# Kernel optimization log

Measured on AMD Instinct MI355X. Metric: run time of the kernel, lower is better.

The kernel has to match this reference:

```python
import jax, jax.numpy as jnp
from jax import lax
import numpy as np

B, S, E, HID = 16, 7, 64, 64
RES = (64, 64); D = RES[0] * RES[1]
XLOW, XHIGH = -0.5, 0.5
RLOW, RHIGH = float(np.sqrt(0.01)), float(np.sqrt(0.05))
PIXEL_MULT = 1.0; N_ITER = 3; TSOFT = 1.0 / float(np.sqrt(E))

def _build_grid():
    ranges = [np.linspace(XLOW, XHIGH, r) for r in RES]
    g = np.stack(np.meshgrid(*ranges, indexing='xy'), axis=-1)
    g = g.reshape(RES[0], RES[1], -1).reshape(1, -1, 2)
    return jnp.asarray(g, dtype=jnp.float32)

ABS_GRID = _build_grid()  # [1, D, 2]

def _ln(x, g, b):
    m = jnp.mean(x, -1, keepdims=True)
    v = jnp.mean(jnp.square(x - m), -1, keepdims=True)
    return (x - m) * lax.rsqrt(v + 1e-5) * g + b

def _forward(data, slot_noise, pos_rand, conv0_w, conv0_b, conv1_w, conv1_b, conv2_w, conv2_b,
             dataN_g, dataN_b, queryN_g, queryN_b, toK_w, toK_b, toV_w, toV_b, dense_w, dense_b,
             mlp1_w, mlp1_b, mlp2_w, mlp2_b, gru_wih, gru_whh, gru_bih, gru_bhh,
             alpha1_w, alpha1_b, alpha2_w, alpha2_b, final1_w, final1_b, final2_w, final2_b,
             slots_mu, slots_logsigma):
    dn = ('NCHW', 'OIHW', 'NCHW')
    def conv(x, w, b):
        return lax.conv_general_dilated(x, w, (1, 1), 'SAME', dimension_numbers=dn) + b[None, :, None, None]
    # CNN encoder: Conv-ReLU x3, 'same' padding, k=5
    x = jax.nn.relu(conv(data, conv0_w, conv0_b))
    x = jax.nn.relu(conv(x, conv1_w, conv1_b))
    x = jax.nn.relu(conv(x, conv2_w, conv2_b))
    enc = x.transpose(0, 2, 3, 1).reshape(B, D, HID)
    enc = _ln(enc, dataN_g, dataN_b)

    queries = slots_mu + jnp.exp(slots_logsigma) * slot_noise  # [B,S,E]
    # init_slots: faithful replication (source indexes the SLOT dim, and swaps rlow/rhigh)
    pos_scale = pos_rand.at[:, :2, :].add(-0.5)
    pos_scale = pos_scale.at[:, -1, :].set((RLOW - RHIGH) * pos_rand[:, -1, :] + RHIGH)

    encK = enc @ toK_w + toK_b  # [B,D,E]
    encV = enc @ toV_w + toV_b

    def init_mlp(y):
        y = _ln(y, queryN_g, queryN_b)
        return jax.nn.relu(y @ mlp1_w + mlp1_b) @ mlp2_w + mlp2_b

    def get_kv(ps):
        # per-slot relative grid: [B,S,D,2]
        rel = (ABS_GRID[:, None] - ps[:, :, None, :2]) / ps[:, :, -1][:, :, None, None]
        eg = PIXEL_MULT * (rel @ dense_w + dense_b)  # [B,S,D,E]
        return init_mlp(encK[:, None] + eg), init_mlp(encV[:, None] + eg)

    def att_wts(q, k):
        logits = jnp.einsum('bse,bsde->bsd', q, k) * TSOFT
        att = jax.nn.softmax(logits, axis=1)  # softmax over slots
        wts = att / jnp.sum(att, -1, keepdims=True) + 1e-8
        return att, wts

    def update_frames(wts):
        new_pos = jnp.einsum('bsd,de->bse', wts, ABS_GRID[0])  # [B,S,2]
        d2 = jnp.sum(jnp.square(ABS_GRID[:, None] - new_pos[:, :, None]), -1)  # [B,S,D]
        new_scale = jnp.sqrt(jnp.einsum('bsd,bsd->bs', wts, d2))
        return jnp.concatenate([new_pos, new_scale[..., None]], -1)

    def gru(xg, h):
        gi = xg @ gru_wih.T + gru_bih
        gh = h @ gru_whh.T + gru_bhh
        ir, iz, inn = jnp.split(gi, 3, -1)
        hr, hz, hn = jnp.split(gh, 3, -1)
        r = jax.nn.sigmoid(ir + hr)
        z = jax.nn.sigmoid(iz + hz)
        n = jnp.tanh(inn + r * hn)
        return (1.0 - z) * n + z * h

    for _ in range(N_ITER):
        keys, vals = get_kv(pos_scale)
        att, wts = att_wts(_ln(queries, queryN_g, queryN_b), keys)
        pos_scale = update_frames(wts)
        upd = jnp.einsum('bsd,bsde->bse', wts, vals)
        queries = gru(upd.reshape(-1, E), queries.reshape(-1, E)).reshape(B, S, E)

    keys, _ = get_kv(pos_scale)
    att, wts = att_wts(_ln(queries, queryN_g, queryN_b), keys)
    nps = update_frames(wts)
    alpha = jax.nn.sigmoid(jax.nn.relu(queries @ alpha1_w + alpha1_b) @ alpha2_w + alpha2_b)
    slot_feat = jax.nn.relu(queries @ final1_w + final1_b) @ final2_w + final2_b + nps
    return queries, att, slot_feat, alpha

def setup_inputs() -> dict:
    ks = jax.random.split(jax.random.key(0), 20)
    f32 = jnp.float32
    def rn(i, shape, s):
        return jax.random.normal(ks[i], shape, f32) * s
    inp = dict(
        data=jax.random.normal(ks[0], (B, 1, RES[0], RES[1]), f32),
        slot_noise=jax.random.normal(ks[1], (B, S, E), f32),
        pos_rand=jax.random.uniform(ks[2], (B, S, 3), dtype=f32),
        conv0_w=rn(3, (HID, 1, 5, 5), 0.2), conv0_b=jnp.zeros(HID, f32),
        conv1_w=rn(4, (HID, HID, 5, 5), 0.025), conv1_b=jnp.zeros(HID, f32),
        conv2_w=rn(5, (HID, HID, 5, 5), 0.025), conv2_b=jnp.zeros(HID, f32),
        dataN_g=jnp.ones(HID, f32), dataN_b=jnp.zeros(HID, f32),
        queryN_g=jnp.ones(E, f32), queryN_b=jnp.zeros(E, f32),
        toK_w=rn(6, (HID, E), 0.125), toK_b=jnp.zeros(E, f32),
        toV_w=rn(7, (HID, E), 0.125), toV_b=jnp.zeros(E, f32),
        dense_w=rn(8, (2, E), 0.7), dense_b=jnp.zeros(E, f32),
        mlp1_w=rn(9, (E, E), 0.125), mlp1_b=jnp.zeros(E, f32),
        mlp2_w=rn(10, (E, E), 0.125), mlp2_b=jnp.zeros(E, f32),
        gru_wih=rn(11, (3 * E, E), 0.125), gru_whh=rn(12, (3 * E, E), 0.125),
        gru_bih=jnp.zeros(3 * E, f32), gru_bhh=jnp.zeros(3 * E, f32),
        alpha1_w=rn(13, (E, 32), 0.125), alpha1_b=jnp.zeros(32, f32),
        alpha2_w=rn(14, (32, 1), 0.18), alpha2_b=jnp.zeros(1, f32),
        final1_w=rn(15, (E, HID), 0.125), final1_b=jnp.zeros(HID, f32),
        final2_w=rn(16, (HID, 3), 0.125), final2_b=jnp.zeros(3, f32),
        slots_mu=rn(17, (1, 1, E), 1.0),
        slots_logsigma=rn(18, (1, 1, E), 0.01),
    )
    return inp

def reference(data, slot_noise, pos_rand, conv0_w, conv0_b, conv1_w, conv1_b, conv2_w, conv2_b,
              dataN_g, dataN_b, queryN_g, queryN_b, toK_w, toK_b, toV_w, toV_b, dense_w, dense_b,
              mlp1_w, mlp1_b, mlp2_w, mlp2_b, gru_wih, gru_whh, gru_bih, gru_bhh,
              alpha1_w, alpha1_b, alpha2_w, alpha2_b, final1_w, final1_b, final2_w, final2_b,
              slots_mu, slots_logsigma):
    return _forward(data, slot_noise, pos_rand, conv0_w, conv0_b, conv1_w, conv1_b, conv2_w, conv2_b,
                    dataN_g, dataN_b, queryN_g, queryN_b, toK_w, toK_b, toV_w, toV_b, dense_w, dense_b,
                    mlp1_w, mlp1_b, mlp2_w, mlp2_b, gru_wih, gru_whh, gru_bih, gru_bhh,
                    alpha1_w, alpha1_b, alpha2_w, alpha2_b, final1_w, final1_b, final2_w, final2_b,
                    slots_mu, slots_logsigma)
```

## Files before the change

### kernel.cpp

```cpp
#include <hip/hip_runtime.h>
#include <cmath>


#define RLOW_F 0.1f
#define RHIGH_F 0.22360679774997896f
#define W0CONST 1.00004096f
#define SR2 704.3386243f

typedef __attribute__((ext_vector_type(8))) __bf16 bf16x8;
typedef __attribute__((ext_vector_type(4))) float f32x4;

__device__ __forceinline__ float wsum64(float v){
  #pragma unroll
  for (int off = 32; off > 0; off >>= 1) v += __shfl_xor(v, off, 64);
  return v;
}
__device__ __forceinline__ float rdlane(float v, int l){
  return __int_as_float(__builtin_amdgcn_readlane(__float_as_int(v), l));
}
__device__ __forceinline__ unsigned short bf16bits(float v){
  __bf16 h = (__bf16)v;
  return *reinterpret_cast<unsigned short*>(&h);
}

__device__ __forceinline__ void pp_core(int row, int e, float qv,
    float px, float py, float sc,
    const float* __restrict__ qg_, const float* __restrict__ qb_,
    const float* __restrict__ dw, const float* __restrict__ db,
    const float* __restrict__ mlp2w, const float* __restrict__ mlp2b,
    float* __restrict__ absc, float* __restrict__ w2qc){
  float m = wsum64(qv) * (1.f/64.f);
  float d = qv - m;
  float var = wsum64(d*d) * (1.f/64.f);
  float qlnv = d * (1.0f/sqrtf(var + 1e-5f)) * qg_[e] + qb_[e];
  float A  = dw[e]      / sc;
  float Bv = dw[64 + e] / sc;
  absc[row*192 + e]       = A;
  absc[row*192 + 64 + e]  = Bv;
  absc[row*192 + 128 + e] = db[e] - px*A - py*Bv;
  float acc = 0.f;
  const float* wrow = mlp2w + e*64;
  for (int j = 0; j < 64; j++) acc = fmaf(wrow[j], rdlane(qlnv, j), acc);
  w2qc[row*68 + e] = acc;
  float c2 = wsum64(mlp2b[e] * qlnv);
  if (e == 0) w2qc[row*68 + 64] = c2;
}

__global__ void k_prep(const float* __restrict__ noise, const float* __restrict__ prand,
                       const float* __restrict__ mu, const float* __restrict__ logsig,
                       const float* __restrict__ qg_, const float* __restrict__ qb_,
                       const float* __restrict__ dw, const float* __restrict__ db,
                       const float* __restrict__ mlp2w, const float* __restrict__ mlp2b,
                       float* __restrict__ queries, float* __restrict__ ps,
                       float* __restrict__ absc, float* __restrict__ w2qc,
                       float* __restrict__ accF, float* __restrict__ upd){
  int row = blockIdx.x;
  int e = threadIdx.x;
  int s = row % 7;
  float qv = mu[e] + expf(logsig[e]) * noise[row*64 + e];
  queries[row*64 + e] = qv;
  upd[row*64 + e] = 0.f;
  if (e < 4) accF[row*4 + e] = 0.f;
  float pv = 0.f;
  if (e < 3){
    float pr = prand[row*3 + e];
    if (s < 2)       pv = pr - 0.5f;
    else if (s == 6) pv = (RLOW_F - RHIGH_F)*pr + RHIGH_F;
    else             pv = pr;
    ps[row*3 + e] = pv;
  }
  float px = rdlane(pv, 0), py = rdlane(pv, 1), sc = rdlane(pv, 2);
  pp_core(row, e, qv, px, py, sc, qg_, qb_, dw, db, mlp2w, mlp2b, absc, w2qc);
}

__global__ __launch_bounds__(256) void k_conv0(const float* __restrict__ in,
                        const float* __restrict__ w, const float* __restrict__ bias,
                        unsigned short* __restrict__ out){
  int bi = blockIdx.x; int b = bi >> 6; int y = bi & 63;
  int t = threadIdx.x; int lane = t & 63; int xg = t >> 6;
  __shared__ float s_in[5*68];
  __shared__ float s_w[64*25];
  __shared__ float s_out[64*65];
  for (int i = t; i < 1600; i += 256) s_w[i] = w[i];
  for (int i = t; i < 340; i += 256){
    int r = i / 68, cx = i % 68;
    int yy = y + r - 2, gx = cx - 2;
    float v = 0.f;
    if (yy >= 0 && yy < 64 && gx >= 0 && gx < 64) v = in[(b*64 + yy)*64 + gx];
    s_in[r*68 + cx] = v;
  }
  __syncthreads();
  int o = lane;
  float bvv = bias[o];
  float acc[16];
  #pragma unroll
  for (int k = 0; k < 16; k++) acc[k] = bvv;
  #pragma unroll
  for (int ky = 0; ky < 5; ky++){
    float rv[20];
    const float4* p = reinterpret_cast<const float4*>(&s_in[ky*68 + xg*16]);
    #pragma unroll
    for (int q = 0; q < 5; q++){ float4 f = p[q]; rv[q*4]=f.x; rv[q*4+1]=f.y; rv[q*4+2]=f.z; rv[q*4+3]=f.w; }
    #pragma unroll
    for (int kx = 0; kx < 5; kx++){
      float wv = s_w[o*25 + ky*5 + kx];
      #pragma unroll
      for (int k = 0; k < 16; k++) acc[k] = fmaf(rv[k+kx], wv, acc[k]);
    }
  }
  #pragma unroll
  for (int k = 0; k < 16; k++) s_out[o*65 + xg*16 + k] = fmaxf(acc[k], 0.f);
  __syncthreads();
  for (int i = t; i < 4096; i += 256){
    int px = i >> 6, ch = i & 63;
    out[((size_t)(b*64 + y)*64 + px)*64 + ch] = bf16bits(s_out[ch*65 + px]);
  }
}

__global__ void k_packconv(const float* __restrict__ w, unsigned short* __restrict__ out){
  int idx = blockIdx.x*256 + threadIdx.x;
  if (idx >= 102400) return;
  int j = idx & 7;
  int l = (idx >> 3) & 63;
  int frag = idx >> 9;
  int nt = frag & 3;
  int ks = (frag >> 2) % 10;
  int dy = frag / 40;
  int q = l >> 4, cr = l & 15;
  int k = ks*32 + q*8 + j;
  int kx = k >> 6, ch = k & 63;
  int n = nt*16 + cr;
  out[idx] = bf16bits(w[((n*64 + ch)*5 + dy)*5 + kx]);
}

__global__ __launch_bounds__(256) void k_convm(const unsigned short* __restrict__ in_bf,
                        const unsigned short* __restrict__ wpack,
                        const float* __restrict__ bias,
                        const float* __restrict__ lng, const float* __restrict__ lnb,
                        unsigned short* __restrict__ out_bf, float* __restrict__ out_f,
                        int mode){
  int bi = blockIdx.x;
  int b = bi >> 4; int yg = bi & 15;
  int t = threadIdx.x; int wv = t >> 6; int l = t & 63;
  int q = l >> 4, cr = l & 15;
  int p0 = wv*16;

  __shared__ char lds[8*68*144];

  for (int ri = 0; ri < 8; ri++){
    int yy = yg*4 + ri - 2;
    bool rok = (yy >= 0 && yy < 64);
    const uint4* src = reinterpret_cast<const uint4*>(in_bf + (size_t)(b*64 + yy)*64*64);
    for (int i = t; i < 544; i += 256){
      int px = i >> 3, c8 = i & 7;
      uint4 v = {0u,0u,0u,0u};
      int gx = px - 2;
      if (rok && gx >= 0 && gx < 64) v = src[gx*8 + c8];
      *reinterpret_cast<uint4*>(&lds[ri*9792 + px*144 + c8*16]) = v;
    }
  }
  __syncthreads();

  f32x4 acc[4][4];
  #pragma unroll
  for (int r = 0; r < 4; r++)
    #pragma unroll
    for (int nt = 0; nt < 4; nt++) acc[r][nt] = (f32x4){0.f,0.f,0.f,0.f};

  const bf16x8* wp = reinterpret_cast<const bf16x8*>(wpack);
  for (int dy = 0; dy < 5; dy++){
    for (int ks = 0; ks < 10; ks++){
      bf16x8 Bf[4];
      int fbase = (dy*10 + ks)*4;
      #pragma unroll
      for (int nt = 0; nt < 4; nt++) Bf[nt] = wp[(fbase + nt)*64 + l];
      int aoff = (p0 + cr + (ks >> 1))*144 + (ks & 1)*64 + q*16;
      #pragma unroll
      for (int r = 0; r < 4; r++){
        bf16x8 a = *reinterpret_cast<const bf16x8*>(&lds[(r + dy)*9792 + aoff]);
        #pragma unroll
        for (int nt = 0; nt < 4; nt++)
          acc[r][nt] = __builtin_amdgcn_mfma_f32_16x16x32_bf16(a, Bf[nt], acc[r][nt], 0, 0, 0);
      }
    }
  }

  float bvv[4];
  #pragma unroll
  for (int nt = 0; nt < 4; nt++) bvv[nt] = bias[nt*16 + cr];

  if (mode == 0){
    #pragma unroll
    for (int r = 0; r < 4; r++){
      int y = yg*4 + r;
      #pragma unroll
      for (int reg = 0; reg < 4; reg++){
        int p = p0 + q*4 + reg;
        size_t base = ((size_t)(b*64 + y)*64 + p)*64;
        #pragma unroll
        for (int nt = 0; nt < 4; nt++)
          out_bf[base + nt*16 + cr] = bf16bits(fmaxf(acc[r][nt][reg] + bvv[nt], 0.f));
      }
    }
  } else {
    float gv[4], bb[4];
    #pragma unroll
    for (int nt = 0; nt < 4; nt++){ gv[nt] = lng[nt*16 + cr]; bb[nt] = lnb[nt*16 + cr]; }
    #pragma unroll
    for (int r = 0; r < 4; r++){
      int y = yg*4 + r;
      #pragma unroll
      for (int reg = 0; reg < 4; reg++){
        int p = p0 + q*4 + reg;
        float v[4]; float s1 = 0.f, s2 = 0.f;
        #pragma unroll
        for (int nt = 0; nt < 4; nt++){
          v[nt] = fmaxf(acc[r][nt][reg] + bvv[nt], 0.f);
          s1 += v[nt]; s2 += v[nt]*v[nt];
        }
        #pragma unroll
        for (int m = 1; m < 16; m <<= 1){ s1 += __shfl_xor(s1, m, 64); s2 += __shfl_xor(s2, m, 64); }
        float mean = s1 * (1.f/64.f);
        float var  = s2 * (1.f/64.f) - mean*mean;
        float rstd = 1.0f/sqrtf(var + 1e-5f);
        size_t base = ((size_t)b*4096 + y*64 + p)*64;
        #pragma unroll
        for (int nt = 0; nt < 4; nt++)
          out_f[base + nt*16 + cr] = (v[nt] - mean)*rstd*gv[nt] + bb[nt];
      }
    }
  }
}

__global__ void k_packw1(const float* __restrict__ w1, unsigned short* __restrict__ out){
  int idx = blockIdx.x*256 + threadIdx.x;
  int jj = idx & 7;
  int lane = (idx >> 3) & 63;
  int frag = idx >> 9;
  int ks = frag >> 2, nt = frag & 3;
  int q = lane >> 4, cr = lane & 15;
  int k = ks*32 + q*8 + jj;
  int n = nt*16 + cr;
  out[idx] = bf16bits(w1[k*64 + n]);
}

__global__ __launch_bounds__(256) void k_projm(const float* __restrict__ enc,
                       const unsigned short* __restrict__ kpack, const float* __restrict__ bk,
                       const unsigned short* __restrict__ vpack, const float* __restrict__ bvp,
                       unsigned short* __restrict__ K, unsigned short* __restrict__ V){
  int bi = blockIdx.x; int b = bi >> 6; int tile = bi & 63;
  int t = threadIdx.x; int wv = t >> 6; int l = t & 63;
  int q = l >> 4, cr = l & 15;
  int d0 = tile*64 + wv*16;

  const bf16x8* kp = reinterpret_cast<const bf16x8*>(kpack);
  const bf16x8* vp = reinterpret_cast<const bf16x8*>(vpack);
  bf16x8 KB[8], VB[8];
  #pragma unroll
  for (int f = 0; f < 8; f++){ KB[f] = kp[f*64 + l]; VB[f] = vp[f*64 + l]; }

  const float* er = enc + (size_t)(b*4096 + d0 + cr)*64;
  bf16x8 a0, a1;
  #pragma unroll
  for (int h = 0; h < 2; h++){
    const float4* e4 = reinterpret_cast<const float4*>(er + (h ? (32 + q*8) : (q*8)));
    #pragma unroll
    for (int p = 0; p < 2; p++){
      float4 e = e4[p];
      if (h == 0){ a0[p*4+0]=(__bf16)e.x; a0[p*4+1]=(__bf16)e.y; a0[p*4+2]=(__bf16)e.z; a0[p*4+3]=(__bf16)e.w; }
      else       { a1[p*4+0]=(__bf16)e.x; a1[p*4+1]=(__bf16)e.y; a1[p*4+2]=(__bf16)e.z; a1[p*4+3]=(__bf16)e.w; }
    }
  }

  f32x4 zero = {0.f,0.f,0.f,0.f};
  f32x4 aK[4], aV[4];
  #pragma unroll
  for (int nt = 0; nt < 4; nt++){
    aK[nt] = __builtin_amdgcn_mfma_f32_16x16x32_bf16(a0, KB[nt],     zero,   0, 0, 0);
    aK[nt] = __builtin_amdgcn_mfma_f32_16x16x32_bf16(a1, KB[4 + nt], aK[nt], 0, 0, 0);
    aV[nt] = __builtin_amdgcn_mfma_f32_16x16x32_bf16(a0, VB[nt],     zero,   0, 0, 0);
    aV[nt] = __builtin_amdgcn_mfma_f32_16x16x32_bf16(a1, VB[4 + nt], aV[nt], 0, 0, 0);
  }
  #pragma unroll
  for (int nt = 0; nt < 4; nt++){
    float bkv = bk[nt*16 + cr], bvv = bvp[nt*16 + cr];
    #pragma unroll
    for (int reg = 0; reg < 4; reg++){
      size_t base = ((size_t)b*4096 + d0 + q*4 + reg)*64 + nt*16 + cr;
      K[base] = bf16bits(aK[nt][reg] + bkv);
      V[base] = bf16bits(aV[nt][reg] + bvv);
    }
  }
}

__global__ __launch_bounds__(256) void k_attnK(const unsigned short* __restrict__ encX,
     const unsigned short* __restrict__ w1pack, const float* __restrict__ mlp1b,
     const float* __restrict__ absc, const float* __restrict__ qg_,
     const float* __restrict__ qb_, const float* __restrict__ w2qc,
     float* __restrict__ att, float* __restrict__ accF){
  int bi = blockIdx.x;
  int b = bi >> 6, tile = bi & 63;
  int t = threadIdx.x; int wv = t >> 6; int l = t & 63;
  int q = l >> 4, cr = l & 15;
  int m0 = tile*64 + wv*16;
  int drow = m0 + cr;

  __shared__ float s_log[7*64];
  __shared__ float s_absc[7*192];
  __shared__ float s_wq[7*68];
  for (int i = t; i < 1344; i += 256) s_absc[i] = absc[b*7*192 + i];
  for (int i = t; i < 476;  i += 256) s_wq[i]   = w2qc[b*7*68 + i];

  const bf16x8* wp = reinterpret_cast<const bf16x8*>(w1pack);
  bf16x8 Bf[8];
  #pragma unroll
  for (int f = 0; f < 8; f++) Bf[f] = wp[f*64 + l];

  const unsigned short* er = encX + (size_t)(b*4096 + drow)*64;
  float gx = -0.5f + (float)(drow & 63) * (1.f/63.f);
  float gy = -0.5f + (float)((drow >> 6) & 63) * (1.f/63.f);
  float xb[16], gq[16], bq[16];
  {
    bf16x8 ea = *reinterpret_cast<const bf16x8*>(er + q*8);
    bf16x8 eb = *reinterpret_cast<const bf16x8*>(er + 32 + q*8);
    #pragma unroll
    for (int i = 0; i < 8; i++){ xb[i] = (float)ea[i]; xb[8+i] = (float)eb[i]; }
  }
  #pragma unroll
  for (int h = 0; h < 2; h++){
    int fb = h ? (32 + q*8) : (q*8);
    const float4* g4 = reinterpret_cast<const float4*>(qg_ + fb);
    const float4* b4 = reinterpret_cast<const float4*>(qb_ + fb);
    #pragma unroll
    for (int p = 0; p < 2; p++){
      float4 gg = g4[p], bb = b4[p];
      int o = h*8 + p*4;
      gq[o+0]=gg.x; gq[o+1]=gg.y; gq[o+2]=gg.z; gq[o+3]=gg.w;
      bq[o+0]=bb.x; bq[o+1]=bb.y; bq[o+2]=bb.z; bq[o+3]=bb.w;
    }
  }
  float b1v[4];
  #pragma unroll
  for (int nt = 0; nt < 4; nt++) b1v[nt] = mlp1b[nt*16 + cr];
  __syncthreads();

  for (int s = 0; s < 7; s++){
    const float* Ac = s_absc + s*192;
    float x[16];
    #pragma unroll
    for (int h = 0; h < 2; h++){
      int fb = h ? (32 + q*8) : (q*8);
      const float4* A4 = reinterpret_cast<const float4*>(Ac + fb);
      const float4* B4 = reinterpret_cast<const float4*>(Ac + 64 + fb);
      const float4* C4 = reinterpret_cast<const float4*>(Ac + 128 + fb);
      #pragma unroll
      for (int p = 0; p < 2; p++){
        float4 Av = A4[p], Bv = B4[p], Cv = C4[p];
        int o = h*8 + p*4;
        x[o+0] = xb[o+0] + gx*Av.x + gy*Bv.x + Cv.x;
        x[o+1] = xb[o+1] + gx*Av.y + gy*Bv.y + Cv.y;
        x[o+2] = xb[o+2] + gx*Av.z + gy*Bv.z + Cv.z;
        x[o+3] = xb[o+3] + gx*Av.w + gy*Bv.w + Cv.w;
      }
    }
    float sum = 0.f;
    #pragma unroll
    for (int k = 0; k < 16; k++) sum += x[k];
    sum += __shfl_xor(sum, 16, 64); sum += __shfl_xor(sum, 32, 64);
    float m = sum * (1.f/64.f);
    float v = 0.f;
    #pragma unroll
    for (int k = 0; k < 16; k++){ float dd = x[k] - m; v += dd*dd; }
    v += __shfl_xor(v, 16, 64); v += __shfl_xor(v, 32, 64);
    float rstd = 1.0f/sqrtf(v * (1.f/64.f) + 1e-5f);

    bf16x8 a0, a1;
    #pragma unroll
    for (int k = 0; k < 8; k++)  a0[k] = (__bf16)((x[k]   - m)*rstd*gq[k]   + bq[k]);
    #pragma unroll
    for (int k = 0; k < 8; k++)  a1[k] = (__bf16)((x[8+k] - m)*rstd*gq[8+k] + bq[8+k]);

    f32x4 zero = {0.f, 0.f, 0.f, 0.f};
    f32x4 acc[4];
    #pragma unroll
    for (int nt = 0; nt < 4; nt++){
      acc[nt] = __builtin_amdgcn_mfma_f32_16x16x32_bf16(a0, Bf[nt],     zero,    0, 0, 0);
      acc[nt] = __builtin_amdgcn_mfma_f32_16x16x32_bf16(a1, Bf[4 + nt], acc[nt], 0, 0, 0);
    }

    float c2 = s_wq[s*68 + 64];
    float p[4] = {0.f, 0.f, 0.f, 0.f};
    #pragma unroll
    for (int nt = 0; nt < 4; nt++){
      float wqv = s_wq[s*68 + nt*16 + cr];
      #pragma unroll
      for (int reg = 0; reg < 4; reg++){
        float y = fmaxf(acc[nt][reg] + b1v[nt], 0.f);
        p[reg] = fmaf(y, wqv, p[reg]);
      }
    }
    #pragma unroll
    for (int reg = 0; reg < 4; reg++){
      #pragma unroll
      for (int off = 1; off < 16; off <<= 1) p[reg] += __shfl_xor(p[reg], off, 64);
    }
    if (cr == 0){
      #pragma unroll
      for (int reg = 0; reg < 4; reg++)
        s_log[s*64 + wv*16 + q*4 + reg] = (p[reg] + c2) * 0.125f;
    }
  }
  __syncthreads();

  if (t < 64){
    float lv[7];
    #pragma unroll
    for (int s = 0; s < 7; s++) lv[s] = s_log[s*64 + t];
    float mx = lv[0];
    #pragma unroll
    for (int s = 1; s < 7; s++) mx = fmaxf(mx, lv[s]);
    float sm = 0.f;
    #pragma unroll
    for (int s = 0; s < 7; s++){ lv[s] = expf(lv[s] - mx); sm += lv[s]; }
    float inv = 1.0f / sm;
    #pragma unroll
    for (int s = 0; s < 7; s++){
      float a = lv[s] * inv;
      s_log[s*64 + t] = a;
      att[(size_t)(b*7+s)*4096 + tile*64 + t] = a;
    }
  }
  __syncthreads();

  if (t < 224){
    int s = t >> 5, r = t & 31;
    float a1 = s_log[s*64 + r];
    float a2 = s_log[s*64 + r + 32];
    float gx1 = -0.5f + (float)r * (1.f/63.f);
    float gx2 = -0.5f + (float)(r + 32) * (1.f/63.f);
    float gyc = -0.5f + (float)tile * (1.f/63.f);
    float gy2c = gyc*gyc;
    float w0 = a1 + a2;
    float w1 = a1*gx1 + a2*gx2;
    float w2 = w0*gyc;
    float w3 = a1*(gx1*gx1 + gy2c) + a2*(gx2*gx2 + gy2c);
    #pragma unroll
    for (int m = 1; m < 32; m <<= 1){
      w0 += __shfl_xor(w0, m, 64);
      w1 += __shfl_xor(w1, m, 64);
      w2 += __shfl_xor(w2, m, 64);
      w3 += __shfl_xor(w3, m, 64);
    }
    if (r == 0){
      atomicAdd(&accF[(b*7+s)*4 + 0], w0);
      atomicAdd(&accF[(b*7+s)*4 + 1], w1);
      atomicAdd(&accF[(b*7+s)*4 + 2], w2);
      atomicAdd(&accF[(b*7+s)*4 + 3], w3);
    }
  }
}

__global__ __launch_bounds__(256) void k_attnV(const unsigned short* __restrict__ encX,
     const unsigned short* __restrict__ w1pack, const float* __restrict__ mlp1b,
     const float* __restrict__ absc, const float* __restrict__ qg_,
     const float* __restrict__ qb_, const float* __restrict__ att,
     const float* __restrict__ accF, float* __restrict__ upd){
  int bi = blockIdx.x;
  int b = bi >> 6, tile = bi & 63;
  int t = threadIdx.x; int wv = t >> 6; int l = t & 63;
  int q = l >> 4, cr = l & 15;
  int m0 = tile*64 + wv*16;
  int drow = m0 + cr;

  __shared__ float s_absc[7*192];
  __shared__ float s_att[7*64];
  __shared__ float s_upd[7*64];
  __shared__ float s_inv[7];
  for (int i = t; i < 1344; i += 256) s_absc[i] = absc[b*7*192 + i];
  for (int i = t; i < 448;  i += 256){
    s_att[i] = att[(size_t)(b*7 + (i >> 6))*4096 + tile*64 + (i & 63)];
    s_upd[i] = 0.f;
  }
  if (t < 7) s_inv[t] = 1.0f / accF[(b*7 + t)*4];

  const bf16x8* wp = reinterpret_cast<const bf16x8*>(w1pack);
  bf16x8 Bf[8];
  #pragma unroll
  for (int f = 0; f < 8; f++) Bf[f] = wp[f*64 + l];

  const unsigned short* er = encX + (size_t)(b*4096 + drow)*64;
  float gx = -0.5f + (float)(drow & 63) * (1.f/63.f);
  float gy = -0.5f + (float)((drow >> 6) & 63) * (1.f/63.f);
  float xb[16], gq[16], bq[16];
  {
    bf16x8 ea = *reinterpret_cast<const bf16x8*>(er + q*8);
    bf16x8 eb = *reinterpret_cast<const bf16x8*>(er + 32 + q*8);
    #pragma unroll
    for (int i = 0; i < 8; i++){ xb[i] = (float)ea[i]; xb[8+i] = (float)eb[i]; }
  }
  #pragma unroll
  for (int h = 0; h < 2; h++){
    int fb = h ? (32 + q*8) : (q*8);
    const float4* g4 = reinterpret_cast<const float4*>(qg_ + fb);
    const float4* b4 = reinterpret_cast<const float4*>(qb_ + fb);
    #pragma unroll
    for (int p = 0; p < 2; p++){
      float4 gg = g4[p], bb = b4[p];
      int o = h*8 + p*4;
      gq[o+0]=gg.x; gq[o+1]=gg.y; gq[o+2]=gg.z; gq[o+3]=gg.w;
      bq[o+0]=bb.x; bq[o+1]=bb.y; bq[o+2]=bb.z; bq[o+3]=bb.w;
    }
  }
  float b1v[4];
  #pragma unroll
  for (int nt = 0; nt < 4; nt++) b1v[nt] = mlp1b[nt*16 + cr];
  __syncthreads();

  for (int s = 0; s < 7; s++){
    const float* Ac = s_absc + s*192;
    float x[16];
    #pragma unroll
    for (int h = 0; h < 2; h++){
      int fb = h ? (32 + q*8) : (q*8);
      const float4* A4 = reinterpret_cast<const float4*>(Ac + fb);
      const float4* B4 = reinterpret_cast<const float4*>(Ac + 64 + fb);
      const float4* C4 = reinterpret_cast<const float4*>(Ac + 128 + fb);
      #pragma unroll
      for (int p = 0; p < 2; p++){
        float4 Av = A4[p], Bv = B4[p], Cv = C4[p];
        int o = h*8 + p*4;
        x[o+0] = xb[o+0] + gx*Av.x + gy*Bv.x + Cv.x;
        x[o+1] = xb[o+1] + gx*Av.y + gy*Bv.y + Cv.y;
        x[o+2] = xb[o+2] + gx*Av.z + gy*Bv.z + Cv.z;
        x[o+3] = xb[o+3] + gx*Av.w + gy*Bv.w + Cv.w;
      }
    }
    float sum = 0.f;
    #pragma unroll
    for (int k = 0; k < 16; k++) sum += x[k];
    sum += __shfl_xor(sum, 16, 64); sum += __shfl_xor(sum, 32, 64);
    float m = sum * (1.f/64.f);
    float v = 0.f;
    #pragma unroll
    for (int k = 0; k < 16; k++){ float dd = x[k] - m; v += dd*dd; }
    v += __shfl_xor(v, 16, 64); v += __shfl_xor(v, 32, 64);
    float rstd = 1.0f/sqrtf(v * (1.f/64.f) + 1e-5f);

    bf16x8 a0, a1;
    #pragma unroll
    for (int k = 0; k < 8; k++)  a0[k] = (__bf16)((x[k]   - m)*rstd*gq[k]   + bq[k]);
    #pragma unroll
    for (int k = 0; k < 8; k++)  a1[k] = (__bf16)((x[8+k] - m)*rstd*gq[8+k] + bq[8+k]);

    f32x4 zero = {0.f, 0.f, 0.f, 0.f};
    f32x4 acc[4];
    #pragma unroll
    for (int nt = 0; nt < 4; nt++){
      acc[nt] = __builtin_amdgcn_mfma_f32_16x16x32_bf16(a0, Bf[nt],     zero,    0, 0, 0);
      acc[nt] = __builtin_amdgcn_mfma_f32_16x16x32_bf16(a1, Bf[4 + nt], acc[nt], 0, 0, 0);
    }

    float rsa = s_inv[s];
    float wr[4];
    #pragma unroll
    for (int reg = 0; reg < 4; reg++)
      wr[reg] = fmaf(s_att[s*64 + wv*16 + q*4 + reg], rsa, 1e-8f);
    float pc[4];
    #pragma unroll
    for (int nt = 0; nt < 4; nt++){
      pc[nt] = 0.f;
      #pragma unroll
      for (int reg = 0; reg < 4; reg++)
        pc[nt] = fmaf(wr[reg], fmaxf(acc[nt][reg] + b1v[nt], 0.f), pc[nt]);
    }
    #pragma unroll
    for (int nt = 0; nt < 4; nt++){
      pc[nt] += __shfl_xor(pc[nt], 16, 64);
      pc[nt] += __shfl_xor(pc[nt], 32, 64);
    }
    if (q == 0){
      #pragma unroll
      for (int nt = 0; nt < 4; nt++)
        atomicAdd(&s_upd[s*64 + nt*16 + cr], pc[nt]);
    }
  }
  __syncthreads();
  for (int i = t; i < 448; i += 256)
    atomicAdd(&upd[b*448 + i], s_upd[i]);
}

__global__ void k_gru(float* __restrict__ upd, float* __restrict__ queries,
                      const float* __restrict__ wih, const float* __restrict__ whh,
                      const float* __restrict__ bih, const float* __restrict__ bhh,
                      const float* __restrict__ mlp2w, const float* __restrict__ mlp2b,
                      float* __restrict__ accF, float* __restrict__ ps,
                      const float* __restrict__ qg_, const float* __restrict__ qb_,
                      const float* __restrict__ dw, const float* __restrict__ db,
                      float* __restrict__ absc, float* __restrict__ w2qc){
  int row = blockIdx.x; int t = threadIdx.x;
  __shared__ float us[64], hs[64], xs[64], gis[192], ghs[192];
  __shared__ float s_ps3[3];
  if (t < 64){ us[t] = upd[row*64 + t]; hs[t] = queries[row*64 + t]; }
  if (t == 64){
    float sa = accF[row*4+0];
    float ax = accF[row*4+1], ay = accF[row*4+2], ar2 = accF[row*4+3];
    float isa = 1.0f/sa;
    float Wx = ax*isa, Wy = ay*isa;
    float Wg = ar2*isa + 1e-8f*SR2;
    float s2 = Wg - (Wx*Wx + Wy*Wy)*(2.f - W0CONST);
    s_ps3[0] = Wx; s_ps3[1] = Wy; s_ps3[2] = sqrtf(fmaxf(s2, 0.f));
  }
  __syncthreads();
  if (t < 64){
    float a = W0CONST * mlp2b[t];
    for (int i = 0; i < 64; i++) a = fmaf(us[i], mlp2w[i*64 + t], a);
    xs[t] = a;
  }
  __syncthreads();
  float gi = bih[t], gh = bhh[t];
  for (int e = 0; e < 64; e++){
    gi = fmaf(wih[t*64 + e], xs[e], gi);
    gh = fmaf(whh[t*64 + e], hs[e], gh);
  }
  gis[t] = gi; ghs[t] = gh;
  __syncthreads();
  if (t < 64){
    float r = 1.0f/(1.0f + expf(-(gis[t]      + ghs[t])));
    float z = 1.0f/(1.0f + expf(-(gis[64+t]   + ghs[64+t])));
    float n = tanhf(gis[128+t] + r*ghs[128+t]);
    float newq = (1.0f - z)*n + z*hs[t];
    queries[row*64 + t] = newq;
    upd[row*64 + t] = 0.f;
    if (t < 4) accF[row*4 + t] = 0.f;
    if (t < 3) ps[row*3 + t] = s_ps3[t];
    pp_core(row, t, newq, s_ps3[0], s_ps3[1], s_ps3[2],
            qg_, qb_, dw, db, mlp2w, mlp2b, absc, w2qc);
  }
}

__global__ void k_final(const float* __restrict__ queries, const float* __restrict__ accF,
                        const float* __restrict__ a1w, const float* __restrict__ a1b,
                        const float* __restrict__ a2w, const float* __restrict__ a2b,
                        const float* __restrict__ f1w, const float* __restrict__ f1b,
                        const float* __restrict__ f2w, const float* __restrict__ f2b,
                        float* __restrict__ out){
  int bs = blockIdx.x; int e = threadIdx.x;
  __shared__ float qs[64], hf[64], ha[32];
  float q = queries[bs*64 + e];
  qs[e] = q;
  out[bs*64 + e] = q;
  __syncthreads();
  float accf = f1b[e];
  for (int i = 0; i < 64; i++) accf = fmaf(qs[i], f1w[i*64 + e], accf);
  hf[e] = fmaxf(accf, 0.f);
  if (e < 32){
    float acca = a1b[e];
    for (int i = 0; i < 64; i++) acca = fmaf(qs[i], a1w[i*32 + e], acca);
    ha[e] = fmaxf(acca, 0.f);
  }
  __syncthreads();
  if (e < 3){
    float sf = f2b[e];
    for (int o = 0; o < 64; o++) sf = fmaf(hf[o], f2w[o*3 + e], sf);
    float sa = accF[bs*4+0], ax = accF[bs*4+1], ay = accF[bs*4+2], ar2 = accF[bs*4+3];
    float isa = 1.0f/sa;
    float Wx = ax*isa, Wy = ay*isa;
    float Wg = ar2*isa + 1e-8f*SR2;
    float s2 = Wg - (Wx*Wx + Wy*Wy)*(2.f - W0CONST);
    float nv = (e == 0) ? Wx : ((e == 1) ? Wy : sqrtf(fmaxf(s2, 0.f)));
    out[465920 + bs*3 + e] = sf + nv;
  }
  if (e == 32){
    float al = a2b[0];
    for (int o = 0; o < 32; o++) al = fmaf(ha[o], a2w[o], al);
    out[466256 + bs] = 1.0f/(1.0f + expf(-al));
  }
}

extern "C" void kernel_launch(void* const* d_in, const int* in_sizes, int n_in,
                              void* d_out, int out_size, void* d_ws, size_t ws_size,
                              hipStream_t stream){
  const float* data        = (const float*)d_in[0];
  const float* slot_noise  = (const float*)d_in[1];
  const float* pos_rand    = (const float*)d_in[2];
  const float* conv0_w     = (const float*)d_in[3];
  const float* conv0_b     = (const float*)d_in[4];
  const float* conv1_w     = (const float*)d_in[5];
  const float* conv1_b     = (const float*)d_in[6];
  const float* conv2_w     = (const float*)d_in[7];
  const float* conv2_b     = (const float*)d_in[8];
  const float* dataN_g     = (const float*)d_in[9];
  const float* dataN_b     = (const float*)d_in[10];
  const float* queryN_g    = (const float*)d_in[11];
  const float* queryN_b    = (const float*)d_in[12];
  const float* toK_w       = (const float*)d_in[13];
  const float* toK_b       = (const float*)d_in[14];
  const float* toV_w       = (const float*)d_in[15];
  const float* toV_b       = (const float*)d_in[16];
  const float* dense_w     = (const float*)d_in[17];
  const float* dense_b     = (const float*)d_in[18];
  const float* mlp1_w      = (const float*)d_in[19];
  const float* mlp1_b      = (const float*)d_in[20];
  const float* mlp2_w      = (const float*)d_in[21];
  const float* mlp2_b      = (const float*)d_in[22];
  const float* gru_wih     = (const float*)d_in[23];
  const float* gru_whh     = (const float*)d_in[24];
  const float* gru_bih     = (const float*)d_in[25];
  const float* gru_bhh     = (const float*)d_in[26];
  const float* alpha1_w    = (const float*)d_in[27];
  const float* alpha1_b    = (const float*)d_in[28];
  const float* alpha2_w    = (const float*)d_in[29];
  const float* alpha2_b    = (const float*)d_in[30];
  const float* final1_w    = (const float*)d_in[31];
  const float* final1_b    = (const float*)d_in[32];
  const float* final2_w    = (const float*)d_in[33];
  const float* final2_b    = (const float*)d_in[34];
  const float* slots_mu    = (const float*)d_in[35];
  const float* slots_lsig  = (const float*)d_in[36];

  float* ws   = (float*)d_ws;
  float* bufA = ws;
  float* bufB = bufA + 4194304;
  float* bufC = bufB + 4194304;
  float* attw = bufC + 4194304;
  float* queries = attw + 458752;
  float* ps   = queries + 7168;
  float* absc = ps + 512;
  float* accF = absc + 21504;
  float* upd  = accF + 512;
  float* w2qc = upd + 7168;
  unsigned short* w1pack = (unsigned short*)(w2qc + 7616);
  unsigned short* kpack  = w1pack + 4096;
  unsigned short* vpack  = kpack + 4096;
  unsigned short* wp1    = vpack + 4096;
  unsigned short* wp2    = wp1 + 102400;

  unsigned short* c0_bf = (unsigned short*)bufA;
  unsigned short* c1_bf = (unsigned short*)bufC;
  float* enc = bufB;
  unsigned short* encK = (unsigned short*)bufA;
  unsigned short* encV = (unsigned short*)bufC;

  float* outq   = (float*)d_out;
  float* outatt = outq + 7168;

  k_prep<<<112, 64, 0, stream>>>(slot_noise, pos_rand, slots_mu, slots_lsig,
                                 queryN_g, queryN_b, dense_w, dense_b, mlp2_w, mlp2_b,
                                 queries, ps, absc, w2qc, accF, upd);
  k_packw1<<<16, 256, 0, stream>>>(mlp1_w, w1pack);
  k_packw1<<<16, 256, 0, stream>>>(toK_w, kpack);
  k_packw1<<<16, 256, 0, stream>>>(toV_w, vpack);
  k_packconv<<<400, 256, 0, stream>>>(conv1_w, wp1);
  k_packconv<<<400, 256, 0, stream>>>(conv2_w, wp2);
  k_conv0<<<1024, 256, 0, stream>>>(data, conv0_w, conv0_b, c0_bf);
  k_convm<<<256, 256, 0, stream>>>(c0_bf, wp1, conv1_b, nullptr, nullptr, c1_bf, nullptr, 0);
  k_convm<<<256, 256, 0, stream>>>(c1_bf, wp2, conv2_b, dataN_g, dataN_b, nullptr, enc, 1);
  k_projm<<<1024, 256, 0, stream>>>(enc, kpack, toK_b, vpack, toV_b, encK, encV);

  for (int p = 0; p < 4; p++){
    float* attp = (p == 3) ? outatt : attw;
    k_attnK<<<1024, 256, 0, stream>>>(encK, w1pack, mlp1_b, absc, queryN_g, queryN_b,
                                      w2qc, attp, accF);
    if (p < 3){
      k_attnV<<<1024, 256, 0, stream>>>(encV, w1pack, mlp1_b, absc, queryN_g, queryN_b,
                                        attp, accF, upd);
      k_gru<<<112, 192, 0, stream>>>(upd, queries, gru_wih, gru_whh, gru_bih, gru_bhh,
                                     mlp2_w, mlp2_b, accF, ps, queryN_g, queryN_b,
                                     dense_w, dense_b, absc, w2qc);
    }
  }
  k_final<<<112, 64, 0, stream>>>(queries, accF,
                                  alpha1_w, alpha1_b, alpha2_w, alpha2_b,
                                  final1_w, final1_b, final2_w, final2_b, outq);
}
```

Before: 535.2 us.

## Stage MLP1 weights in LDS and process slot pairs in attention kernels

Both attention kernels now copy the packed MLP1 weight fragments into shared memory instead of holding eight bf16x8 fragments in registers per lane. They also process two slots per loop iteration to interleave independent MFMA chains, and compute layernorm variance in a single pass from sum and sum of squares. A launch bound of 4 blocks per SM is added to push register use down for higher occupancy. The trade-offs are LDS reads per MFMA, one duplicated wasted slot computation on the final odd iteration, and slightly less numerically stable variance.

```diff
diff --git a/kernel.cpp b/kernel.cpp
--- a/kernel.cpp
+++ b/kernel.cpp
@@ -293,7 +293,7 @@
   }
 }
 
-__global__ __launch_bounds__(256) void k_attnK(const unsigned short* __restrict__ encX,
+__global__ __launch_bounds__(256, 4) void k_attnK(const unsigned short* __restrict__ encX,
      const unsigned short* __restrict__ w1pack, const float* __restrict__ mlp1b,
      const float* __restrict__ absc, const float* __restrict__ qg_,
      const float* __restrict__ qb_, const float* __restrict__ w2qc,
@@ -308,13 +308,14 @@
   __shared__ float s_log[7*64];
   __shared__ float s_absc[7*192];
   __shared__ float s_wq[7*68];
+  __shared__ unsigned short s_w1[4096];
   for (int i = t; i < 1344; i += 256) s_absc[i] = absc[b*7*192 + i];
   for (int i = t; i < 476;  i += 256) s_wq[i]   = w2qc[b*7*68 + i];
-
-  const bf16x8* wp = reinterpret_cast<const bf16x8*>(w1pack);
-  bf16x8 Bf[8];
-  #pragma unroll
-  for (int f = 0; f < 8; f++) Bf[f] = wp[f*64 + l];
+  {
+    const uint4* g = reinterpret_cast<const uint4*>(w1pack);
+    uint4* d = reinterpret_cast<uint4*>(s_w1);
+    for (int i = t; i < 512; i += 256) d[i] = g[i];
+  }
 
   const unsigned short* er = encX + (size_t)(b*4096 + drow)*64;
   float gx = -0.5f + (float)(drow & 63) * (1.f/63.f);
@@ -344,70 +345,113 @@
   for (int nt = 0; nt < 4; nt++) b1v[nt] = mlp1b[nt*16 + cr];
   __syncthreads();
 
-  for (int s = 0; s < 7; s++){
-    const float* Ac = s_absc + s*192;
-    float x[16];
-    #pragma unroll
-    for (int h = 0; h < 2; h++){
-      int fb = h ? (32 + q*8) : (q*8);
-      const float4* A4 = reinterpret_cast<const float4*>(Ac + fb);
-      const float4* B4 = reinterpret_cast<const float4*>(Ac + 64 + fb);
-      const float4* C4 = reinterpret_cast<const float4*>(Ac + 128 + fb);
-      #pragma unroll
-      for (int p = 0; p < 2; p++){
-        float4 Av = A4[p], Bv = B4[p], Cv = C4[p];
-        int o = h*8 + p*4;
-        x[o+0] = xb[o+0] + gx*Av.x + gy*Bv.x + Cv.x;
-        x[o+1] = xb[o+1] + gx*Av.y + gy*Bv.y + Cv.y;
-        x[o+2] = xb[o+2] + gx*Av.z + gy*Bv.z + Cv.z;
-        x[o+3] = xb[o+3] + gx*Av.w + gy*Bv.w + Cv.w;
-      }
-    }
-    float sum = 0.f;
-    #pragma unroll
-    for (int k = 0; k < 16; k++) sum += x[k];
-    sum += __shfl_xor(sum, 16, 64); sum += __shfl_xor(sum, 32, 64);
-    float m = sum * (1.f/64.f);
-    float v = 0.f;
-    #pragma unroll
-    for (int k = 0; k < 16; k++){ float dd = x[k] - m; v += dd*dd; }
-    v += __shfl_xor(v, 16, 64); v += __shfl_xor(v, 32, 64);
-    float rstd = 1.0f/sqrtf(v * (1.f/64.f) + 1e-5f);
-
-    bf16x8 a0, a1;
-    #pragma unroll
-    for (int k = 0; k < 8; k++)  a0[k] = (__bf16)((x[k]   - m)*rstd*gq[k]   + bq[k]);
-    #pragma unroll
-    for (int k = 0; k < 8; k++)  a1[k] = (__bf16)((x[8+k] - m)*rstd*gq[8+k] + bq[8+k]);
-
-    f32x4 zero = {0.f, 0.f, 0.f, 0.f};
-    f32x4 acc[4];
+  const bf16x8* wl = reinterpret_cast<const bf16x8*>(s_w1);
+  f32x4 zero = {0.f, 0.f, 0.f, 0.f};
+
+  for (int sp = 0; sp < 4; sp++){
+    int s0 = sp*2;
+    int np = (sp == 3) ? 1 : 2;
+    int sB = (np == 2) ? s0 + 1 : s0;
+    float x0[16], x1[16];
+    float s1a = 0.f, s2a = 0.f, s1b = 0.f, s2b = 0.f;
+    {
+      const float* Ac = s_absc + s0*192;
+      #pragma unroll
+      for (int h = 0; h < 2; h++){
+        int fb = h ? (32 + q*8) : (q*8);
+        const float4* A4 = reinterpret_cast<const float4*>(Ac + fb);
+        const float4* B4 = reinterpret_cast<const float4*>(Ac + 64 + fb);
+        const float4* C4 = reinterpret_cast<const float4*>(Ac + 128 + fb);
+        #pragma unroll
+        for (int p = 0; p < 2; p++){
+          float4 Av = A4[p], Bv = B4[p], Cv = C4[p];
+          int o = h*8 + p*4;
+          x0[o+0] = xb[o+0] + gx*Av.x + gy*Bv.x + Cv.x;
+          x0[o+1] = xb[o+1] + gx*Av.y + gy*Bv.y + Cv.y;
+          x0[o+2] = xb[o+2] + gx*Av.z + gy*Bv.z + Cv.z;
+          x0[o+3] = xb[o+3] + gx*Av.w + gy*Bv.w + Cv.w;
+        }
+      }
+      #pragma unroll
+      for (int k = 0; k < 16; k++){ s1a += x0[k]; s2a = fmaf(x0[k], x0[k], s2a); }
+    }
+    {
+      const float* Ac = s_absc + sB*192;
+      #pragma unroll
+      for (int h = 0; h < 2; h++){
+        int fb = h ? (32 + q*8) : (q*8);
+        const float4* A4 = reinterpret_cast<const float4*>(Ac + fb);
+        const float4* B4 = reinterpret_cast<const float4*>(Ac + 64 + fb);
+        const float4* C4 = reinterpret_cast<const float4*>(Ac + 128 + fb);
+        #pragma unroll
+        for (int p = 0; p < 2; p++){
+          float4 Av = A4[p], Bv = B4[p], Cv = C4[p];
+          int o = h*8 + p*4;
+          x1[o+0] = xb[o+0] + gx*Av.x + gy*Bv.x + Cv.x;
+          x1[o+1] = xb[o+1] + gx*Av.y + gy*Bv.y + Cv.y;
+          x1[o+2] = xb[o+2] + gx*Av.z + gy*Bv.z + Cv.z;
+          x1[o+3] = xb[o+3] + gx*Av.w + gy*Bv.w + Cv.w;
+        }
+      }
+      #pragma unroll
+      for (int k = 0; k < 16; k++){ s1b += x1[k]; s2b = fmaf(x1[k], x1[k], s2b); }
+    }
+    s1a += __shfl_xor(s1a, 16, 64); s2a += __shfl_xor(s2a, 16, 64);
+    s1b += __shfl_xor(s1b, 16, 64); s2b += __shfl_xor(s2b, 16, 64);
+    s1a += __shfl_xor(s1a, 32, 64); s2a += __shfl_xor(s2a, 32, 64);
+    s1b += __shfl_xor(s1b, 32, 64); s2b += __shfl_xor(s2b, 32, 64);
+    float mA = s1a*(1.f/64.f);
+    float rA = 1.0f/sqrtf(s2a*(1.f/64.f) - mA*mA + 1e-5f);
+    float mB = s1b*(1.f/64.f);
+    float rB = 1.0f/sqrtf(s2b*(1.f/64.f) - mB*mB + 1e-5f);
+
+    bf16x8 a00, a01, a10, a11;
+    #pragma unroll
+    for (int k = 0; k < 8; k++){
+      a00[k] = (__bf16)((x0[k]    - mA)*rA*gq[k]   + bq[k]);
+      a01[k] = (__bf16)((x0[8+k]  - mA)*rA*gq[8+k] + bq[8+k]);
+      a10[k] = (__bf16)((x1[k]    - mB)*rB*gq[k]   + bq[k]);
+      a11[k] = (__bf16)((x1[8+k]  - mB)*rB*gq[8+k] + bq[8+k]);
+    }
+
+    f32x4 acc0[4], acc1[4];
     #pragma unroll
     for (int nt = 0; nt < 4; nt++){
-      acc[nt] = __builtin_amdgcn_mfma_f32_16x16x32_bf16(a0, Bf[nt],     zero,    0, 0, 0);
-      acc[nt] = __builtin_amdgcn_mfma_f32_16x16x32_bf16(a1, Bf[4 + nt], acc[nt], 0, 0, 0);
-    }
-
-    float c2 = s_wq[s*68 + 64];
-    float p[4] = {0.f, 0.f, 0.f, 0.f};
+      bf16x8 w0 = wl[nt*64 + l];
+      bf16x8 w1f = wl[(4 + nt)*64 + l];
+      acc0[nt] = __builtin_amdgcn_mfma_f32_16x16x32_bf16(a00, w0,  zero,     0, 0, 0);
+      acc0[nt] = __builtin_amdgcn_mfma_f32_16x16x32_bf16(a01, w1f, acc0[nt], 0, 0, 0);
+      acc1[nt] = __builtin_amdgcn_mfma_f32_16x16x32_bf16(a10, w0,  zero,     0, 0, 0);
+      acc1[nt] = __builtin_amdgcn_mfma_f32_16x16x32_bf16(a11, w1f, acc1[nt], 0, 0, 0);
+    }
+
+    float p0[4] = {0.f,0.f,0.f,0.f}, p1[4] = {0.f,0.f,0.f,0.f};
     #pragma unroll
     for (int nt = 0; nt < 4; nt++){
-      float wqv = s_wq[s*68 + nt*16 + cr];
+      float wq0 = s_wq[s0*68 + nt*16 + cr];
+      float wq1 = s_wq[sB*68 + nt*16 + cr];
       #pragma unroll
       for (int reg = 0; reg < 4; reg++){
-        float y = fmaxf(acc[nt][reg] + b1v[nt], 0.f);
-        p[reg] = fmaf(y, wqv, p[reg]);
-      }
-    }
-    #pragma unroll
-    for (int reg = 0; reg < 4; reg++){
-      #pragma unroll
-      for (int off = 1; off < 16; off <<= 1) p[reg] += __shfl_xor(p[reg], off, 64);
+        p0[reg] = fmaf(fmaxf(acc0[nt][reg] + b1v[nt], 0.f), wq0, p0[reg]);
+        p1[reg] = fmaf(fmaxf(acc1[nt][reg] + b1v[nt], 0.f), wq1, p1[reg]);
+      }
+    }
+    #pragma unroll
+    for (int off = 1; off < 16; off <<= 1){
+      #pragma unroll
+      for (int reg = 0; reg < 4; reg++){
+        p0[reg] += __shfl_xor(p0[reg], off, 64);
+        p1[reg] += __shfl_xor(p1[reg], off, 64);
+      }
     }
     if (cr == 0){
-      #pragma unroll
-      for (int reg = 0; reg < 4; reg++)
-        s_log[s*64 + wv*16 + q*4 + reg] = (p[reg] + c2) * 0.125f;
+      float c20 = s_wq[s0*68 + 64];
+      float c21 = s_wq[sB*68 + 64];
+      #pragma unroll
+      for (int reg = 0; reg < 4; reg++){
+        s_log[s0*64 + wv*16 + q*4 + reg] = (p0[reg] + c20) * 0.125f;
+        if (np == 2) s_log[sB*64 + wv*16 + q*4 + reg] = (p1[reg] + c21) * 0.125f;
+      }
     }
   }
   __syncthreads();
@@ -460,7 +504,7 @@
   }
 }
 
-__global__ __launch_bounds__(256) void k_attnV(const unsigned short* __restrict__ encX,
+__global__ __launch_bounds__(256, 4) void k_attnV(const unsigned short* __restrict__ encX,
      const unsigned short* __restrict__ w1pack, const float* __restrict__ mlp1b,
      const float* __restrict__ absc, const float* __restrict__ qg_,
      const float* __restrict__ qb_, const float* __restrict__ att,
@@ -476,17 +520,18 @@
   __shared__ float s_att[7*64];
   __shared__ float s_upd[7*64];
   __shared__ float s_inv[7];
+  __shared__ unsigned short s_w1[4096];
   for (int i = t; i < 1344; i += 256) s_absc[i] = absc[b*7*192 + i];
   for (int i = t; i < 448;  i += 256){
     s_att[i] = att[(size_t)(b*7 + (i >> 6))*4096 + tile*64 + (i & 63)];
     s_upd[i] = 0.f;
   }
   if (t < 7) s_inv[t] = 1.0f / accF[(b*7 + t)*4];
-
-  const bf16x8* wp = reinterpret_cast<const bf16x8*>(w1pack);
-  bf16x8 Bf[8];
-  #pragma unroll
-  for (int f = 0; f < 8; f++) Bf[f] = wp[f*64 + l];
+  {
+    const uint4* g = reinterpret_cast<const uint4*>(w1pack);
+    uint4* d = reinterpret_cast<uint4*>(s_w1);
+    for (int i = t; i < 512; i += 256) d[i] = g[i];
+  }
 
   const unsigned short* er = encX + (size_t)(b*4096 + drow)*64;
   float gx = -0.5f + (float)(drow & 63) * (1.f/63.f);
@@ -516,72 +561,116 @@
   for (int nt = 0; nt < 4; nt++) b1v[nt] = mlp1b[nt*16 + cr];
   __syncthreads();
 
-  for (int s = 0; s < 7; s++){
-    const float* Ac = s_absc + s*192;
-    float x[16];
-    #pragma unroll
-    for (int h = 0; h < 2; h++){
-      int fb = h ? (32 + q*8) : (q*8);
-      const float4* A4 = reinterpret_cast<const float4*>(Ac + fb);
-      const float4* B4 = reinterpret_cast<const float4*>(Ac + 64 + fb);
-      const float4* C4 = reinterpret_cast<const float4*>(Ac + 128 + fb);
-      #pragma unroll
-      for (int p = 0; p < 2; p++){
-        float4 Av = A4[p], Bv = B4[p], Cv = C4[p];
-        int o = h*8 + p*4;
-        x[o+0] = xb[o+0] + gx*Av.x + gy*Bv.x + Cv.x;
-        x[o+1] = xb[o+1] + gx*Av.y + gy*Bv.y + Cv.y;
-        x[o+2] = xb[o+2] + gx*Av.z + gy*Bv.z + Cv.z;
-        x[o+3] = xb[o+3] + gx*Av.w + gy*Bv.w + Cv.w;
-      }
-    }
-    float sum = 0.f;
-    #pragma unroll
-    for (int k = 0; k < 16; k++) sum += x[k];
-    sum += __shfl_xor(sum, 16, 64); sum += __shfl_xor(sum, 32, 64);
-    float m = sum * (1.f/64.f);
-    float v = 0.f;
-    #pragma unroll
-    for (int k = 0; k < 16; k++){ float dd = x[k] - m; v += dd*dd; }
-    v += __shfl_xor(v, 16, 64); v += __shfl_xor(v, 32, 64);
-    float rstd = 1.0f/sqrtf(v * (1.f/64.f) + 1e-5f);
-
-    bf16x8 a0, a1;
-    #pragma unroll
-    for (int k = 0; k < 8; k++)  a0[k] = (__bf16)((x[k]   - m)*rstd*gq[k]   + bq[k]);
-    #pragma unroll
-    for (int k = 0; k < 8; k++)  a1[k] = (__bf16)((x[8+k] - m)*rstd*gq[8+k] + bq[8+k]);
-
-    f32x4 zero = {0.f, 0.f, 0.f, 0.f};
-    f32x4 acc[4];
+  const bf16x8* wl = reinterpret_cast<const bf16x8*>(s_w1);
+  f32x4 zero = {0.f, 0.f, 0.f, 0.f};
+
+  for (int sp = 0; sp < 4; sp++){
+    int s0 = sp*2;
+    int np = (sp == 3) ? 1 : 2;
+    int sB = (np == 2) ? s0 + 1 : s0;
+    float x0[16], x1[16];
+    float s1a = 0.f, s2a = 0.f, s1b = 0.f, s2b = 0.f;
+    {
+      const float* Ac = s_absc + s0*192;
+      #pragma unroll
+      for (int h = 0; h < 2; h++){
+        int fb = h ? (32 + q*8) : (q*8);
+        const float4* A4 = reinterpret_cast<const float4*>(Ac + fb);
+        const float4* B4 = reinterpret_cast<const float4*>(Ac + 64 + fb);
+        const float4* C4 = reinterpret_cast<const float4*>(Ac + 128 + fb);
+        #pragma unroll
+        for (int p = 0; p < 2; p++){
+          float4 Av = A4[p], Bv = B4[p], Cv = C4[p];
+          int o = h*8 + p*4;
+          x0[o+0] = xb[o+0] + gx*Av.x + gy*Bv.x + Cv.x;
+          x0[o+1] = xb[o+1] + gx*Av.y + gy*Bv.y + Cv.y;
+          x0[o+2] = xb[o+2] + gx*Av.z + gy*Bv.z + Cv.z;
+          x0[o+3] = xb[o+3] + gx*Av.w + gy*Bv.w + Cv.w;
+        }
+      }
+      #pragma unroll
+      for (int k = 0; k < 16; k++){ s1a += x0[k]; s2a = fmaf(x0[k], x0[k], s2a); }
+    }
+    {
+      const float* Ac = s_absc + sB*192;
+      #pragma unroll
+      for (int h = 0; h < 2; h++){
+        int fb = h ? (32 + q*8) : (q*8);
+        const float4* A4 = reinterpret_cast<const float4*>(Ac + fb);
+        const float4* B4 = reinterpret_cast<const float4*>(Ac + 64 + fb);
+        const float4* C4 = reinterpret_cast<const float4*>(Ac + 128 + fb);
+        #pragma unroll
+        for (int p = 0; p < 2; p++){
+          float4 Av = A4[p], Bv = B4[p], Cv = C4[p];
+          int o = h*8 + p*4;
+          x1[o+0] = xb[o+0] + gx*Av.x + gy*Bv.x + Cv.x;
+          x1[o+1] = xb[o+1] + gx*Av.y + gy*Bv.y + Cv.y;
+          x1[o+2] = xb[o+2] + gx*Av.z + gy*Bv.z + Cv.z;
+          x1[o+3] = xb[o+3] + gx*Av.w + gy*Bv.w + Cv.w;
+        }
+      }
+      #pragma unroll
+      for (int k = 0; k < 16; k++){ s1b += x1[k]; s2b = fmaf(x1[k], x1[k], s2b); }
+    }
+    s1a += __shfl_xor(s1a, 16, 64); s2a += __shfl_xor(s2a, 16, 64);
+    s1b += __shfl_xor(s1b, 16, 64); s2b += __shfl_xor(s2b, 16, 64);
+    s1a += __shfl_xor(s1a, 32, 64); s2a += __shfl_xor(s2a, 32, 64);
+    s1b += __shfl_xor(s1b, 32, 64); s2b += __shfl_xor(s2b, 32, 64);
+    float mA = s1a*(1.f/64.f);
+    float rA = 1.0f/sqrtf(s2a*(1.f/64.f) - mA*mA + 1e-5f);
+    float mB = s1b*(1.f/64.f);
+    float rB = 1.0f/sqrtf(s2b*(1.f/64.f) - mB*mB + 1e-5f);
+
+    bf16x8 a00, a01, a10, a11;
+    #pragma unroll
+    for (int k = 0; k < 8; k++){
+      a00[k] = (__bf16)((x0[k]    - mA)*rA*gq[k]   + bq[k]);
+      a01[k] = (__bf16)((x0[8+k]  - mA)*rA*gq[8+k] + bq[8+k]);
+      a10[k] = (__bf16)((x1[k]    - mB)*rB*gq[k]   + bq[k]);
+      a11[k] = (__bf16)((x1[8+k]  - mB)*rB*gq[8+k] + bq[8+k]);
+    }
+
+    f32x4 acc0[4], acc1[4];
     #pragma unroll
     for (int nt = 0; nt < 4; nt++){
-      acc[nt] = __builtin_amdgcn_mfma_f32_16x16x32_bf16(a0, Bf[nt],     zero,    0, 0, 0);
-      acc[nt] = __builtin_amdgcn_mfma_f32_16x16x32_bf16(a1, Bf[4 + nt], acc[nt], 0, 0, 0);
-    }
-
-    float rsa = s_inv[s];
-    float wr[4];
-    #pragma unroll
-    for (int reg = 0; reg < 4; reg++)
-      wr[reg] = fmaf(s_att[s*64 + wv*16 + q*4 + reg], rsa, 1e-8f);
-    float pc[4];
+      bf16x8 w0 = wl[nt*64 + l];
+      bf16x8 w1f = wl[(4 + nt)*64 + l];
+      acc0[nt] = __builtin_amdgcn_mfma_f32_16x16x32_bf16(a00, w0,  zero,     0, 0, 0);
+      acc0[nt] = __builtin_amdgcn_mfma_f32_16x16x32_bf16(a01, w1f, acc0[nt], 0, 0, 0);
+      acc1[nt] = __builtin_amdgcn_mfma_f32_16x16x32_bf16(a10, w0,  zero,     0, 0, 0);
+      acc1[nt] = __builtin_amdgcn_mfma_f32_16x16x32_bf16(a11, w1f, acc1[nt], 0, 0, 0);
+    }
+
+    float rsa0 = s_inv[s0], rsa1 = s_inv[sB];
+    float wr0[4], wr1[4];
+    #pragma unroll
+    for (int reg = 0; reg < 4; reg++){
+      wr0[reg] = fmaf(s_att[s0*64 + wv*16 + q*4 + reg], rsa0, 1e-8f);
+      wr1[reg] = fmaf(s_att[sB*64 + wv*16 + q*4 + reg], rsa1, 1e-8f);
+    }
+    float pc0[4], pc1[4];
     #pragma unroll
     for (int nt = 0; nt < 4; nt++){
-      pc[nt] = 0.f;
-      #pragma unroll
-      for (int reg = 0; reg < 4; reg++)
-        pc[nt] = fmaf(wr[reg], fmaxf(acc[nt][reg] + b1v[nt], 0.f), pc[nt]);
+      pc0[nt] = 0.f; pc1[nt] = 0.f;
+      #pragma unroll
+      for (int reg = 0; reg < 4; reg++){
+        pc0[nt] = fmaf(wr0[reg], fmaxf(acc0[nt][reg] + b1v[nt], 0.f), pc0[nt]);
+        pc1[nt] = fmaf(wr1[reg], fmaxf(acc1[nt][reg] + b1v[nt], 0.f), pc1[nt]);
+      }
     }
     #pragma unroll
     for (int nt = 0; nt < 4; nt++){
-      pc[nt] += __shfl_xor(pc[nt], 16, 64);
-      pc[nt] += __shfl_xor(pc[nt], 32, 64);
+      pc0[nt] += __shfl_xor(pc0[nt], 16, 64);
+      pc1[nt] += __shfl_xor(pc1[nt], 16, 64);
+      pc0[nt] += __shfl_xor(pc0[nt], 32, 64);
+      pc1[nt] += __shfl_xor(pc1[nt], 32, 64);
     }
     if (q == 0){
       #pragma unroll
-      for (int nt = 0; nt < 4; nt++)
-        atomicAdd(&s_upd[s*64 + nt*16 + cr], pc[nt]);
+      for (int nt = 0; nt < 4; nt++){
+        atomicAdd(&s_upd[s0*64 + nt*16 + cr], pc0[nt]);
+        if (np == 2) atomicAdd(&s_upd[sB*64 + nt*16 + cr], pc1[nt]);
+      }
     }
   }
   __syncthreads();
```

Result: slower. 575.6 us (+7.6%).
